# Performance work log

Hardware: AMD Instinct MI355X
Metric: run time of the kernel (lower is better)

The kernel has to match this reference:

```python
import jax, jax.numpy as jnp
import numpy as np

N, F, E, D, H, G = 65536, 256, 16, 256, 512, 256  # nodes, feat, experts(node_num), emb_dim, hidden_dim, graphs


def setup_inputs() -> dict:
    key = jax.random.key(0)
    ks = jax.random.split(key, 11)
    scale = 0.02
    return {
        "node_fea": jax.random.normal(ks[0], (N, F), jnp.float32),
        "masks": jax.random.uniform(ks[1], (N, F), jnp.float32),
        "node_type": jax.random.randint(ks[2], (N,), 0, E),
        "g_node_id": jnp.sort(jax.random.randint(ks[3], (G,), 0, N)),
        "label": jax.random.randint(ks[4], (G,), 0, 2),
        "W_emb": jax.random.normal(ks[5], (E, F, D), jnp.float32) * scale,
        "b_emb": jax.random.normal(ks[6], (E, D), jnp.float32) * scale,
        "W_hid": jax.random.normal(ks[7], (D, H), jnp.float32) * scale,
        "b_hid": jax.random.normal(ks[8], (H,), jnp.float32) * scale,
        "W_out": jax.random.normal(ks[9], (H, 2), jnp.float32) * scale,
        "b_out": jax.random.normal(ks[10], (2,), jnp.float32) * scale,
    }


def reference(node_fea, masks, node_type, g_node_id, label,
              W_emb, b_emb, W_hid, b_hid, W_out, b_out):
    # --- node_embedding: per-node type-routed linear (grouped GEMM form) ---
    xm = node_fea * masks                                   # [N, F]
    # run every expert densely, then select each node's expert output
    all_emb = jnp.einsum('nf,efd->ned', xm, W_emb) + b_emb[None]   # [N, E, D]
    emb = jnp.take_along_axis(all_emb, node_type[:, None, None], axis=1)[:, 0, :]  # [N, D]
    # --- hidden_fc (dropout in eval mode = identity) ---
    h = emb @ W_hid + b_hid                                 # [N, H]
    # --- pick first node of each batched graph ---
    g_emb = h[g_node_id]                                    # [G, H]
    # --- output layer: Linear + Softmax ---
    probs = jax.nn.softmax(g_emb @ W_out + b_out, axis=-1)  # [G, 2]
    # --- CrossEntropyLoss(reduction='sum') applied to probs (as in source) ---
    logp = jax.nn.log_softmax(probs, axis=-1)
    loss = -jnp.sum(jnp.take_along_axis(logp, label[:, None], axis=1))
    return probs, loss
```

## Files before the change

kernel.cpp:

```cpp
#include <hip/hip_runtime.h>
#include <math.h>

#define NN 65536
#define FF 256
#define EE 16
#define DD 256
#define HH 512
#define GG 256


__global__ __launch_bounds__(256) void fold_kernel(
    const float* __restrict__ W_emb,
    const float* __restrict__ b_emb,
    const float* __restrict__ W_hid,
    const float* __restrict__ b_hid,
    const float* __restrict__ W_out,
    const float* __restrict__ b_out,
    float* __restrict__ fold,
    float* __restrict__ bfold)
{
    __shared__ __align__(16) float wo[2 * HH];
    __shared__ __align__(16) float wtmp[2 * DD];

    const int t = threadIdx.x;
    const int e = blockIdx.x >> 2;
    const int r = blockIdx.x & 3;

    *(float4*)(wo + 4 * t) = *(const float4*)(W_out + 4 * t);
    __syncthreads();

    {
        const float* __restrict__ Wr = W_hid + (size_t)t * HH;
        float a0 = 0.f, a1 = 0.f;
        #pragma unroll 8
        for (int i = 0; i < HH / 4; ++i) {
            const float4 wh = *(const float4*)(Wr + 4 * i);
            const float4 o0 = *(const float4*)(wo + 8 * i);
            const float4 o1 = *(const float4*)(wo + 8 * i + 4);
            a0 = fmaf(wh.x, o0.x, a0);  a1 = fmaf(wh.x, o0.y, a1);
            a0 = fmaf(wh.y, o0.z, a0);  a1 = fmaf(wh.y, o0.w, a1);
            a0 = fmaf(wh.z, o1.x, a0);  a1 = fmaf(wh.z, o1.y, a1);
            a0 = fmaf(wh.w, o1.z, a0);  a1 = fmaf(wh.w, o1.w, a1);
        }
        wtmp[2 * t]     = a0;
        wtmp[2 * t + 1] = a1;
    }
    __syncthreads();

    {
        const int row = (r << 6) + (t >> 2);
        const int d0  = (t & 3) << 6;
        const float* __restrict__ We =
            W_emb + ((size_t)e * FF + row) * DD + d0;
        float z0 = 0.f, z1 = 0.f;
        #pragma unroll 4
        for (int i = 0; i < 16; ++i) {
            const float4 wv = *(const float4*)(We + 4 * i);
            const int d2 = 2 * (d0 + 4 * i);
            z0 = fmaf(wv.x, wtmp[d2 + 0], z0);  z1 = fmaf(wv.x, wtmp[d2 + 1], z1);
            z0 = fmaf(wv.y, wtmp[d2 + 2], z0);  z1 = fmaf(wv.y, wtmp[d2 + 3], z1);
            z0 = fmaf(wv.z, wtmp[d2 + 4], z0);  z1 = fmaf(wv.z, wtmp[d2 + 5], z1);
            z0 = fmaf(wv.w, wtmp[d2 + 6], z0);  z1 = fmaf(wv.w, wtmp[d2 + 7], z1);
        }
        z0 += __shfl_xor(z0, 1, 64);  z1 += __shfl_xor(z1, 1, 64);
        z0 += __shfl_xor(z0, 2, 64);  z1 += __shfl_xor(z1, 2, 64);
        if ((t & 3) == 0)
            *(float2*)(fold + ((size_t)e * FF + row) * 2) = (float2){z0, z1};
    }

    if (r == 0 && t < 64) {
        float c0 = 0.f, c1 = 0.f;
        const float4 bh0 = *(const float4*)(b_hid + 8 * t);
        const float4 bh1 = *(const float4*)(b_hid + 8 * t + 4);
        const int h2 = 16 * t;
        c0 = fmaf(bh0.x, wo[h2 +  0], c0);  c1 = fmaf(bh0.x, wo[h2 +  1], c1);
        c0 = fmaf(bh0.y, wo[h2 +  2], c0);  c1 = fmaf(bh0.y, wo[h2 +  3], c1);
        c0 = fmaf(bh0.z, wo[h2 +  4], c0);  c1 = fmaf(bh0.z, wo[h2 +  5], c1);
        c0 = fmaf(bh0.w, wo[h2 +  6], c0);  c1 = fmaf(bh0.w, wo[h2 +  7], c1);
        c0 = fmaf(bh1.x, wo[h2 +  8], c0);  c1 = fmaf(bh1.x, wo[h2 +  9], c1);
        c0 = fmaf(bh1.y, wo[h2 + 10], c0);  c1 = fmaf(bh1.y, wo[h2 + 11], c1);
        c0 = fmaf(bh1.z, wo[h2 + 12], c0);  c1 = fmaf(bh1.z, wo[h2 + 13], c1);
        c0 = fmaf(bh1.w, wo[h2 + 14], c0);  c1 = fmaf(bh1.w, wo[h2 + 15], c1);
        const float4 be = *(const float4*)(b_emb + e * DD + 4 * t);
        const int d2 = 8 * t;
        c0 = fmaf(be.x, wtmp[d2 + 0], c0);  c1 = fmaf(be.x, wtmp[d2 + 1], c1);
        c0 = fmaf(be.y, wtmp[d2 + 2], c0);  c1 = fmaf(be.y, wtmp[d2 + 3], c1);
        c0 = fmaf(be.z, wtmp[d2 + 4], c0);  c1 = fmaf(be.z, wtmp[d2 + 5], c1);
        c0 = fmaf(be.w, wtmp[d2 + 6], c0);  c1 = fmaf(be.w, wtmp[d2 + 7], c1);
        for (int off = 32; off; off >>= 1) {
            c0 += __shfl_down(c0, off, 64);
            c1 += __shfl_down(c1, off, 64);
        }
        if (t == 0) {
            bfold[2 * e + 0] = c0 + b_out[0];
            bfold[2 * e + 1] = c1 + b_out[1];
        }
    }
}

__global__ __launch_bounds__(1024) void graph_loss_kernel(
    const float* __restrict__ node_fea,
    const float* __restrict__ masks,
    const int*   __restrict__ node_type,
    const int*   __restrict__ g_node_id,
    const int*   __restrict__ label,
    const float* __restrict__ fold,
    const float* __restrict__ bfold,
    float* __restrict__ out)
{
    __shared__ float lterm[GG];
    const int t = threadIdx.x;
    const int w = t >> 6;
    const int l = t & 63;

    #pragma unroll
    for (int p = 0; p < GG / 16; ++p) {
        const int g = (p << 4) + w;
        const int n = g_node_id[g];
        const int e = node_type[n];
        const size_t nb = (size_t)n * FF + (l << 2);
        const float4 x = *(const float4*)(node_fea + nb);
        const float4 m = *(const float4*)(masks + nb);
        const float* fr = fold + e * (FF * 2) + (l << 3);
        const float4 wa = *(const float4*)(fr);
        const float4 wb = *(const float4*)(fr + 4);
        const float x0 = x.x * m.x, x1 = x.y * m.y;
        const float x2 = x.z * m.z, x3 = x.w * m.w;
        float z0 = x0 * wa.x + x1 * wa.z + x2 * wb.x + x3 * wb.z;
        float z1 = x0 * wa.y + x1 * wa.w + x2 * wb.y + x3 * wb.w;
        for (int off = 32; off; off >>= 1) {
            z0 += __shfl_down(z0, off, 64);
            z1 += __shfl_down(z1, off, 64);
        }
        if (l == 0) {
            z0 += bfold[2 * e + 0];
            z1 += bfold[2 * e + 1];
            const float mz = fmaxf(z0, z1);
            const float e0 = expf(z0 - mz), e1 = expf(z1 - mz);
            const float inv = 1.0f / (e0 + e1);
            const float p0 = e0 * inv, p1 = e1 * inv;
            out[2 * g + 0] = p0;
            out[2 * g + 1] = p1;
            const float mp  = fmaxf(p0, p1);
            const float lse = mp + logf(expf(p0 - mp) + expf(p1 - mp));
            lterm[g] = lse - ((label[g] == 0) ? p0 : p1);
        }
    }
    __syncthreads();

    if (t < 64) {
        float v = lterm[t] + lterm[t + 64] + lterm[t + 128] + lterm[t + 192];
        for (int off = 32; off; off >>= 1) v += __shfl_down(v, off, 64);
        if (t == 0) out[2 * GG] = v;
    }
}

extern "C" void kernel_launch(void* const* d_in, const int* in_sizes, int n_in,
                              void* d_out, int out_size, void* d_ws, size_t ws_size,
                              hipStream_t stream) {
    const float* node_fea  = (const float*)d_in[0];
    const float* masks     = (const float*)d_in[1];
    const int*   node_type = (const int*)  d_in[2];
    const int*   g_node_id = (const int*)  d_in[3];
    const int*   label     = (const int*)  d_in[4];
    const float* W_emb     = (const float*)d_in[5];
    const float* b_emb     = (const float*)d_in[6];
    const float* W_hid     = (const float*)d_in[7];
    const float* b_hid     = (const float*)d_in[8];
    const float* W_out     = (const float*)d_in[9];
    const float* b_out     = (const float*)d_in[10];

    float* out   = (float*)d_out;
    float* fold  = (float*)d_ws;
    float* bfold = fold + EE * FF * 2;

    fold_kernel<<<EE * 4, 256, 0, stream>>>(
        W_emb, b_emb, W_hid, b_hid, W_out, b_out, fold, bfold);

    graph_loss_kernel<<<1, 1024, 0, stream>>>(
        node_fea, masks, node_type, g_node_id, label, fold, bfold, out);
}
```

Before: 184.8 us.

## Fuse weight folding and graph loss into one multi-block kernel with grid barriers

Replaces the two-kernel pipeline with a single 64-block persistent kernel that synchronizes through global atomic grid barriers. The W_hid·W_out product is split across waves with coalesced loads and shuffle reductions instead of one serial row per thread. The per-graph logit and loss work is spread over all blocks instead of one block, and the per-expert bias fold is replaced by a per-node b_emb term. This adds a memset plus spin-wait barriers, which depend on all 64 blocks being co-resident.

```diff
diff --git a/kernel.cpp b/kernel.cpp
--- a/kernel.cpp
+++ b/kernel.cpp
@@ -7,134 +7,142 @@
 #define DD 256
 #define HH 512
 #define GG 256
+#define NBLK 64
 
 
-__global__ __launch_bounds__(256) void fold_kernel(
+__device__ __forceinline__ void grid_barrier(int* c, int target) {
+    __syncthreads();
+    if (threadIdx.x == 0) {
+        __hip_atomic_fetch_add(c, 1, __ATOMIC_ACQ_REL, __HIP_MEMORY_SCOPE_AGENT);
+        while (__hip_atomic_load(c, __ATOMIC_ACQUIRE, __HIP_MEMORY_SCOPE_AGENT)
+               < target) {
+            __builtin_amdgcn_s_sleep(1);
+        }
+    }
+    __syncthreads();
+}
+
+__global__ __launch_bounds__(256) void fused_all_kernel(
+    const float* __restrict__ node_fea,
+    const float* __restrict__ masks,
+    const int*   __restrict__ node_type,
+    const int*   __restrict__ g_node_id,
+    const int*   __restrict__ label,
     const float* __restrict__ W_emb,
     const float* __restrict__ b_emb,
     const float* __restrict__ W_hid,
     const float* __restrict__ b_hid,
     const float* __restrict__ W_out,
     const float* __restrict__ b_out,
-    float* __restrict__ fold,
-    float* __restrict__ bfold)
+    float* __restrict__ out,
+    float* __restrict__ ws_f,
+    int*   __restrict__ ws_i)
 {
-    __shared__ __align__(16) float wo[2 * HH];
-    __shared__ __align__(16) float wtmp[2 * DD];
+    __shared__ __align__(16) float lwtmp[2 * DD];
 
     const int t = threadIdx.x;
-    const int e = blockIdx.x >> 2;
-    const int r = blockIdx.x & 3;
+    const int b = blockIdx.x;
+    const int w = t >> 6;
+    const int l = t & 63;
 
-    *(float4*)(wo + 4 * t) = *(const float4*)(W_out + 4 * t);
-    __syncthreads();
+    float* wtmp   = ws_f + 16;
+    float* bconst = ws_f + 528;
+    float* lterm  = ws_f + 544;
+    float* fold   = ws_f + 1024;
+
+    const int g = (b << 2) + w;
+    const int n = g_node_id[g];
+    const int e = node_type[n];
+    const size_t nb = (size_t)n * FF + (l << 2);
+    const float4 x4  = *(const float4*)(node_fea + nb);
+    const float4 m4  = *(const float4*)(masks + nb);
+    const float4 be4 = *(const float4*)(b_emb + e * DD + (l << 2));
 
     {
-        const float* __restrict__ Wr = W_hid + (size_t)t * HH;
-        float a0 = 0.f, a1 = 0.f;
-        #pragma unroll 8
-        for (int i = 0; i < HH / 4; ++i) {
-            const float4 wh = *(const float4*)(Wr + 4 * i);
-            const float4 o0 = *(const float4*)(wo + 8 * i);
-            const float4 o1 = *(const float4*)(wo + 8 * i + 4);
-            a0 = fmaf(wh.x, o0.x, a0);  a1 = fmaf(wh.x, o0.y, a1);
-            a0 = fmaf(wh.y, o0.z, a0);  a1 = fmaf(wh.y, o0.w, a1);
-            a0 = fmaf(wh.z, o1.x, a0);  a1 = fmaf(wh.z, o1.y, a1);
-            a0 = fmaf(wh.w, o1.z, a0);  a1 = fmaf(wh.w, o1.w, a1);
+        const int d = (b << 2) + w;
+        const float* Wr = W_hid + (size_t)d * HH + (l << 3);
+        const float4 h0 = *(const float4*)(Wr);
+        const float4 h1 = *(const float4*)(Wr + 4);
+        const float* Wo = W_out + (l << 4);
+        const float4 o0 = *(const float4*)(Wo);
+        const float4 o1 = *(const float4*)(Wo + 4);
+        const float4 o2 = *(const float4*)(Wo + 8);
+        const float4 o3 = *(const float4*)(Wo + 12);
+        float a0 = h0.x*o0.x + h0.y*o0.z + h0.z*o1.x + h0.w*o1.z
+                 + h1.x*o2.x + h1.y*o2.z + h1.z*o3.x + h1.w*o3.z;
+        float a1 = h0.x*o0.y + h0.y*o0.w + h0.z*o1.y + h0.w*o1.w
+                 + h1.x*o2.y + h1.y*o2.w + h1.z*o3.y + h1.w*o3.w;
+        float c0 = 0.f, c1 = 0.f;
+        if (b == 0 && w == 0) {
+            const float4 bh0 = *(const float4*)(b_hid + (l << 3));
+            const float4 bh1 = *(const float4*)(b_hid + (l << 3) + 4);
+            c0 = bh0.x*o0.x + bh0.y*o0.z + bh0.z*o1.x + bh0.w*o1.z
+               + bh1.x*o2.x + bh1.y*o2.z + bh1.z*o3.x + bh1.w*o3.z;
+            c1 = bh0.x*o0.y + bh0.y*o0.w + bh0.z*o1.y + bh0.w*o1.w
+               + bh1.x*o2.y + bh1.y*o2.w + bh1.z*o3.y + bh1.w*o3.w;
         }
-        wtmp[2 * t]     = a0;
-        wtmp[2 * t + 1] = a1;
+        for (int off = 32; off; off >>= 1) {
+            a0 += __shfl_down(a0, off, 64);
+            a1 += __shfl_down(a1, off, 64);
+            c0 += __shfl_down(c0, off, 64);
+            c1 += __shfl_down(c1, off, 64);
+        }
+        if (l == 0) {
+            wtmp[2 * d]     = a0;
+            wtmp[2 * d + 1] = a1;
+            if (b == 0 && w == 0) {
+                bconst[0] = c0 + b_out[0];
+                bconst[1] = c1 + b_out[1];
+            }
+        }
     }
-    __syncthreads();
+    grid_barrier(ws_i + 0, NBLK);
 
     {
+        *(float2*)(lwtmp + 2 * t) = *(const float2*)(wtmp + 2 * t);
+        __syncthreads();
+
+        const int e2  = b >> 2;
+        const int r   = b & 3;
         const int row = (r << 6) + (t >> 2);
         const int d0  = (t & 3) << 6;
-        const float* __restrict__ We =
-            W_emb + ((size_t)e * FF + row) * DD + d0;
+        const float* We = W_emb + ((size_t)e2 * FF + row) * DD + d0;
         float z0 = 0.f, z1 = 0.f;
         #pragma unroll 4
         for (int i = 0; i < 16; ++i) {
             const float4 wv = *(const float4*)(We + 4 * i);
             const int d2 = 2 * (d0 + 4 * i);
-            z0 = fmaf(wv.x, wtmp[d2 + 0], z0);  z1 = fmaf(wv.x, wtmp[d2 + 1], z1);
-            z0 = fmaf(wv.y, wtmp[d2 + 2], z0);  z1 = fmaf(wv.y, wtmp[d2 + 3], z1);
-            z0 = fmaf(wv.z, wtmp[d2 + 4], z0);  z1 = fmaf(wv.z, wtmp[d2 + 5], z1);
-            z0 = fmaf(wv.w, wtmp[d2 + 6], z0);  z1 = fmaf(wv.w, wtmp[d2 + 7], z1);
+            z0 = fmaf(wv.x, lwtmp[d2 + 0], z0);  z1 = fmaf(wv.x, lwtmp[d2 + 1], z1);
+            z0 = fmaf(wv.y, lwtmp[d2 + 2], z0);  z1 = fmaf(wv.y, lwtmp[d2 + 3], z1);
+            z0 = fmaf(wv.z, lwtmp[d2 + 4], z0);  z1 = fmaf(wv.z, lwtmp[d2 + 5], z1);
+            z0 = fmaf(wv.w, lwtmp[d2 + 6], z0);  z1 = fmaf(wv.w, lwtmp[d2 + 7], z1);
         }
         z0 += __shfl_xor(z0, 1, 64);  z1 += __shfl_xor(z1, 1, 64);
         z0 += __shfl_xor(z0, 2, 64);  z1 += __shfl_xor(z1, 2, 64);
         if ((t & 3) == 0)
-            *(float2*)(fold + ((size_t)e * FF + row) * 2) = (float2){z0, z1};
+            *(float2*)(fold + ((size_t)e2 * FF + row) * 2) = (float2){z0, z1};
     }
+    grid_barrier(ws_i + 1, NBLK);
 
-    if (r == 0 && t < 64) {
-        float c0 = 0.f, c1 = 0.f;
-        const float4 bh0 = *(const float4*)(b_hid + 8 * t);
-        const float4 bh1 = *(const float4*)(b_hid + 8 * t + 4);
-        const int h2 = 16 * t;
-        c0 = fmaf(bh0.x, wo[h2 +  0], c0);  c1 = fmaf(bh0.x, wo[h2 +  1], c1);
-        c0 = fmaf(bh0.y, wo[h2 +  2], c0);  c1 = fmaf(bh0.y, wo[h2 +  3], c1);
-        c0 = fmaf(bh0.z, wo[h2 +  4], c0);  c1 = fmaf(bh0.z, wo[h2 +  5], c1);
-        c0 = fmaf(bh0.w, wo[h2 +  6], c0);  c1 = fmaf(bh0.w, wo[h2 +  7], c1);
-        c0 = fmaf(bh1.x, wo[h2 +  8], c0);  c1 = fmaf(bh1.x, wo[h2 +  9], c1);
-        c0 = fmaf(bh1.y, wo[h2 + 10], c0);  c1 = fmaf(bh1.y, wo[h2 + 11], c1);
-        c0 = fmaf(bh1.z, wo[h2 + 12], c0);  c1 = fmaf(bh1.z, wo[h2 + 13], c1);
-        c0 = fmaf(bh1.w, wo[h2 + 14], c0);  c1 = fmaf(bh1.w, wo[h2 + 15], c1);
-        const float4 be = *(const float4*)(b_emb + e * DD + 4 * t);
-        const int d2 = 8 * t;
-        c0 = fmaf(be.x, wtmp[d2 + 0], c0);  c1 = fmaf(be.x, wtmp[d2 + 1], c1);
-        c0 = fmaf(be.y, wtmp[d2 + 2], c0);  c1 = fmaf(be.y, wtmp[d2 + 3], c1);
-        c0 = fmaf(be.z, wtmp[d2 + 4], c0);  c1 = fmaf(be.z, wtmp[d2 + 5], c1);
-        c0 = fmaf(be.w, wtmp[d2 + 6], c0);  c1 = fmaf(be.w, wtmp[d2 + 7], c1);
-        for (int off = 32; off; off >>= 1) {
-            c0 += __shfl_down(c0, off, 64);
-            c1 += __shfl_down(c1, off, 64);
-        }
-        if (t == 0) {
-            bfold[2 * e + 0] = c0 + b_out[0];
-            bfold[2 * e + 1] = c1 + b_out[1];
-        }
-    }
-}
-
-__global__ __launch_bounds__(1024) void graph_loss_kernel(
-    const float* __restrict__ node_fea,
-    const float* __restrict__ masks,
-    const int*   __restrict__ node_type,
-    const int*   __restrict__ g_node_id,
-    const int*   __restrict__ label,
-    const float* __restrict__ fold,
-    const float* __restrict__ bfold,
-    float* __restrict__ out)
-{
-    __shared__ float lterm[GG];
-    const int t = threadIdx.x;
-    const int w = t >> 6;
-    const int l = t & 63;
-
-    #pragma unroll
-    for (int p = 0; p < GG / 16; ++p) {
-        const int g = (p << 4) + w;
-        const int n = g_node_id[g];
-        const int e = node_type[n];
-        const size_t nb = (size_t)n * FF + (l << 2);
-        const float4 x = *(const float4*)(node_fea + nb);
-        const float4 m = *(const float4*)(masks + nb);
+    {
         const float* fr = fold + e * (FF * 2) + (l << 3);
-        const float4 wa = *(const float4*)(fr);
-        const float4 wb = *(const float4*)(fr + 4);
-        const float x0 = x.x * m.x, x1 = x.y * m.y;
-        const float x2 = x.z * m.z, x3 = x.w * m.w;
-        float z0 = x0 * wa.x + x1 * wa.z + x2 * wb.x + x3 * wb.z;
-        float z1 = x0 * wa.y + x1 * wa.w + x2 * wb.y + x3 * wb.w;
+        const float4 wa  = *(const float4*)(fr);
+        const float4 wb  = *(const float4*)(fr + 4);
+        const float4 wt0 = *(const float4*)(wtmp + (l << 3));
+        const float4 wt1 = *(const float4*)(wtmp + (l << 3) + 4);
+        const float x0 = x4.x * m4.x, x1 = x4.y * m4.y;
+        const float x2 = x4.z * m4.z, x3 = x4.w * m4.w;
+        float z0 = x0*wa.x + x1*wa.z + x2*wb.x + x3*wb.z
+                 + be4.x*wt0.x + be4.y*wt0.z + be4.z*wt1.x + be4.w*wt1.z;
+        float z1 = x0*wa.y + x1*wa.w + x2*wb.y + x3*wb.w
+                 + be4.x*wt0.y + be4.y*wt0.w + be4.z*wt1.y + be4.w*wt1.w;
         for (int off = 32; off; off >>= 1) {
             z0 += __shfl_down(z0, off, 64);
             z1 += __shfl_down(z1, off, 64);
         }
         if (l == 0) {
-            z0 += bfold[2 * e + 0];
-            z1 += bfold[2 * e + 1];
+            z0 += bconst[0];
+            z1 += bconst[1];
             const float mz = fmaxf(z0, z1);
             const float e0 = expf(z0 - mz), e1 = expf(z1 - mz);
             const float inv = 1.0f / (e0 + e1);
@@ -146,9 +154,9 @@
             lterm[g] = lse - ((label[g] == 0) ? p0 : p1);
         }
     }
-    __syncthreads();
+    grid_barrier(ws_i + 2, NBLK);
 
-    if (t < 64) {
+    if (b == 0 && t < 64) {
         float v = lterm[t] + lterm[t + 64] + lterm[t + 128] + lterm[t + 192];
         for (int off = 32; off; off >>= 1) v += __shfl_down(v, off, 64);
         if (t == 0) out[2 * GG] = v;
@@ -170,13 +178,14 @@
     const float* W_out     = (const float*)d_in[9];
     const float* b_out     = (const float*)d_in[10];
 
-    float* out   = (float*)d_out;
-    float* fold  = (float*)d_ws;
-    float* bfold = fold + EE * FF * 2;
+    float* out  = (float*)d_out;
+    float* ws_f = (float*)d_ws;
+    int*   ws_i = (int*)d_ws;
 
-    fold_kernel<<<EE * 4, 256, 0, stream>>>(
-        W_emb, b_emb, W_hid, b_hid, W_out, b_out, fold, bfold);
+    hipMemsetAsync(d_ws, 0, 16, stream);
 
-    graph_loss_kernel<<<1, 1024, 0, stream>>>(
-        node_fea, masks, node_type, g_node_id, label, fold, bfold, out);
+    fused_all_kernel<<<NBLK, 256, 0, stream>>>(
+        node_fea, masks, node_type, g_node_id, label,
+        W_emb, b_emb, W_hid, b_hid, W_out, b_out,
+        out, ws_f, ws_i);
 }
```

After: 156.4 us. 15.4% less time.
